# Optimization experiments

Measured on AMD Instinct MI355X. Metric: run time of the kernel, lower is better.

## Reference

```python
import jax, jax.numpy as jnp
import numpy as np

N_HEADS = 12
LN_EPS = 1e-12


def _attention(x, mask, wq, bq, wk, bk, wv, bv, wo, bo):
    # standard BERT self-attention block (QKV + output projection, no LN here)
    B, S, D = x.shape
    Dh = D // N_HEADS
    q = (x @ wq + bq).reshape(B, S, N_HEADS, Dh)
    k = (x @ wk + bk).reshape(B, S, N_HEADS, Dh)
    v = (x @ wv + bv).reshape(B, S, N_HEADS, Dh)
    scores = jnp.einsum('bqhd,bkhd->bhqk', q, k) / jnp.sqrt(jnp.asarray(Dh, x.dtype))
    scores = scores + mask[:, None, None, :]  # additive mask, broadcast over heads/queries
    a = jax.nn.softmax(scores, axis=-1)
    ctx = jnp.einsum('bhqk,bkhd->bqhd', a, v).reshape(B, S, D)
    return ctx @ wo + bo


def _ffn(x, w1, b1, w2, b2):
    return jax.nn.gelu(x @ w1 + b1, approximate=False) @ w2 + b2


def _switch_ffn(x, wr, br, w1, b1, w2, b2):
    # token-level top-1 Switch FFN: route each token, scale output by max route prob.
    # All sub-experts are computed densely and combined with a one-hot mask so the
    # math is identical to gather/scatter dispatch but jit-friendly.
    B, S, D = x.shape
    E = wr.shape[-1]
    tok = x.reshape(-1, D)  # [N, D]
    p = jax.nn.softmax(tok @ wr + br, axis=-1)  # [N, E]
    pmax = p.max(axis=-1)
    oh = jax.nn.one_hot(p.argmax(axis=-1), E, dtype=tok.dtype)  # [N, E]
    h = jax.nn.gelu(jnp.einsum('nd,edf->enf', tok, w1) + b1[:, None, :], approximate=False)
    y = jnp.einsum('enf,efd->end', h, w2) + b2[:, None, :]  # [E, N, D]
    out = jnp.einsum('ne,end->nd', oh, y) * pmax[:, None]
    return out.reshape(B, S, D)


def setup_inputs() -> dict:
    B, S, D, F, U, E = 16, 128, 768, 3072, 4, 4
    key = jax.random.key(0)
    ks = jax.random.split(key, 20)
    w = lambda i, sh: jax.random.normal(ks[i], sh, dtype=jnp.float32) * 0.02
    z = lambda sh: jnp.zeros(sh, jnp.float32)
    return {
        'x': jax.random.normal(ks[0], (B, S, D), jnp.float32),
        'attn_mask': z((B, S)),
        'sw_w': w(1, (D, U)), 'sw_b': z((U,)),
        'ca_wq': w(2, (D, D)), 'ca_bq': z((D,)),
        'ca_wk': w(3, (D, D)), 'ca_bk': z((D,)),
        'ca_wv': w(4, (D, D)), 'ca_bv': z((D,)),
        'ca_wo': w(5, (D, D)), 'ca_bo': z((D,)),
        'ua_wq': w(6, (U, D, D)), 'ua_bq': z((U, D)),
        'ua_wk': w(7, (U, D, D)), 'ua_bk': z((U, D)),
        'ua_wv': w(8, (U, D, D)), 'ua_bv': z((U, D)),
        'ua_wo': w(9, (U, D, D)), 'ua_bo': z((U, D)),
        'cf_w1': w(10, (D, F)), 'cf_b1': z((F,)),
        'cf_w2': w(11, (F, D)), 'cf_b2': z((D,)),
        'ur_w': w(12, (U, D, E)), 'ur_b': z((U, E)),
        'uf_w1': w(13, (U, E, D, F)), 'uf_b1': z((U, E, F)),
        'uf_w2': w(14, (U, E, F, D)), 'uf_b2': z((U, E, D)),
        'ln_g': jnp.ones((D,), jnp.float32), 'ln_b': z((D,)),
    }


def reference(x, attn_mask, sw_w, sw_b,
              ca_wq, ca_bq, ca_wk, ca_bk, ca_wv, ca_bv, ca_wo, ca_bo,
              ua_wq, ua_bq, ua_wk, ua_bk, ua_wv, ua_bv, ua_wo, ua_bo,
              cf_w1, cf_b1, cf_w2, cf_b2,
              ur_w, ur_b, uf_w1, uf_b1, uf_w2, uf_b2,
              ln_g, ln_b):
    U = sw_w.shape[-1]
    # common attention expert (full batch)
    common_attn = _attention(x, attn_mask, ca_wq, ca_bq, ca_wk, ca_bk, ca_wv, ca_bv, ca_wo, ca_bo)
    # batch-level routing: mean-pool over sequence, softmax + top-1
    route_p = jax.nn.softmax(x.mean(axis=1) @ sw_w + sw_b, axis=-1)  # [B, U]
    pmax = route_p.max(axis=-1)    # [B]
    routes = route_p.argmax(axis=-1)  # [B]
    # unique attention experts: masked dense compute == gather/scatter by batch row
    unique_attn = jnp.zeros_like(x)
    for i in range(U):
        sel = (routes == i)[:, None, None]
        out_i = _attention(x, attn_mask, ua_wq[i], ua_bq[i], ua_wk[i], ua_bk[i],
                           ua_wv[i], ua_bv[i], ua_wo[i], ua_bo[i])
        unique_attn = unique_attn + jnp.where(sel, out_i, jnp.zeros((), x.dtype))
    # note: original multiplies ONLY the unique branch by route_prob_max
    att = common_attn + pmax[:, None, None] * unique_attn
    # unique Switch-FFN experts (token-level top-1 inside each unique expert)
    unique_ffn = jnp.zeros_like(x)
    for i in range(U):
        sel = (routes == i)[:, None, None]
        out_i = _switch_ffn(att, ur_w[i], ur_b[i], uf_w1[i], uf_b1[i], uf_w2[i], uf_b2[i])
        unique_ffn = unique_ffn + jnp.where(sel, out_i, jnp.zeros((), x.dtype))
    common_ffn = _ffn(att, cf_w1, cf_b1, cf_w2, cf_b2)
    ffn_out = common_ffn + unique_ffn  # dropout in eval mode == identity
    y = att + ffn_out
    mu = y.mean(axis=-1, keepdims=True)
    var = y.var(axis=-1, keepdims=True)
    return (y - mu) / jnp.sqrt(var + LN_EPS) * ln_g + ln_b
```

## Files before the change

kernel.cpp:

```cpp
#include <hip/hip_runtime.h>

#define NT 2048
#define Dm 768
#define Fm 3072
#define Bm 16
#define Sm 128
#define Hm 12
#define DHm 64

#define BM 64
#define BM2 128
#define BN 128
#define BK 32

typedef __attribute__((ext_vector_type(8))) short bf16x8;
typedef __attribute__((ext_vector_type(4))) float f32x4;

__device__ __forceinline__ unsigned short f2bf(float f){
  unsigned u = __float_as_uint(f);
  unsigned r = (u + 0x7fffu + ((u>>16)&1u)) >> 16;
  return (unsigned short)r;
}
__device__ __forceinline__ float bf2f(unsigned short h){ return __uint_as_float(((unsigned)h)<<16); }
__device__ __forceinline__ unsigned fsplit2(float x){
  unsigned short h = f2bf(x);
  unsigned short l = f2bf(x - bf2f(h));
  return (unsigned)h | ((unsigned)l << 16);
}
__device__ __forceinline__ float gelu_f(float x){
  return 0.5f*x*(1.0f + erff(x*0.70710678118654752f));
}

__device__ __forceinline__ void mm_tile2(
    const short* __restrict__ Abf, int lda,
    const int* __restrict__ gidx, int m0, int mbound,
    const float* __restrict__ W0, int N, int K, int n0,
    f32x4 acc[4][4])
{
  int lane = threadIdx.x & 63, wv = threadIdx.x >> 6;
  int wm = wv & 1, wn = wv >> 1;
  int oct = lane >> 4, l16 = lane & 15;
  const short* aptr[4];
  #pragma unroll
  for(int fi=0; fi<4; fi++){
    int lr = wm*64 + fi*16 + l16;
    int grow = (lr < mbound) ? (gidx ? gidx[m0 + lr] : (m0 + lr)) : -1;
    aptr[fi] = (grow >= 0) ? (Abf + (size_t)grow*lda + oct*8) : nullptr;
  }
  const float* bptr[4];
  #pragma unroll
  for(int fj=0; fj<4; fj++)
    bptr[fj] = W0 + (size_t)(oct*8)*N + (n0 + wn*64 + fj*16 + l16);

  const bf16x8 zz = {0,0,0,0,0,0,0,0};
  bf16x8 av[4]; float bw[4][8];
  #pragma unroll
  for(int fi=0; fi<4; fi++) av[fi] = aptr[fi] ? *(const bf16x8*)(aptr[fi]) : zz;
  #pragma unroll
  for(int fj=0; fj<4; fj++)
    #pragma unroll
    for(int i=0;i<8;i++) bw[fj][i] = bptr[fj][(size_t)i*N];

  for(int k0=0; k0<K; k0+=BK){
    bf16x8 af[4];
    #pragma unroll
    for(int fi=0; fi<4; fi++) af[fi] = av[fi];
    bf16x8 bfr[4];
    #pragma unroll
    for(int fj=0; fj<4; fj++){
      unsigned o0,o1,o2,o3;
      asm("v_cvt_pk_bf16_f32 %0, %1, %2" : "=v"(o0) : "v"(bw[fj][0]), "v"(bw[fj][1]));
      asm("v_cvt_pk_bf16_f32 %0, %1, %2" : "=v"(o1) : "v"(bw[fj][2]), "v"(bw[fj][3]));
      asm("v_cvt_pk_bf16_f32 %0, %1, %2" : "=v"(o2) : "v"(bw[fj][4]), "v"(bw[fj][5]));
      asm("v_cvt_pk_bf16_f32 %0, %1, %2" : "=v"(o3) : "v"(bw[fj][6]), "v"(bw[fj][7]));
      union{ bf16x8 v; unsigned u[4]; } r;
      r.u[0]=o0; r.u[1]=o1; r.u[2]=o2; r.u[3]=o3;
      bfr[fj] = r.v;
    }
    if(k0+BK < K){
      int kn = k0 + BK;
      #pragma unroll
      for(int fi=0; fi<4; fi++) av[fi] = aptr[fi] ? *(const bf16x8*)(aptr[fi] + kn) : zz;
      #pragma unroll
      for(int fj=0; fj<4; fj++)
        #pragma unroll
        for(int i=0;i<8;i++) bw[fj][i] = bptr[fj][(size_t)(kn + i)*N];
    }
    #pragma unroll
    for(int fi=0; fi<4; fi++)
      #pragma unroll
      for(int fj=0; fj<4; fj++)
        acc[fi][fj] = __builtin_amdgcn_mfma_f32_16x16x32_bf16(af[fi], bfr[fj], acc[fi][fj], 0, 0, 0);
  }
}

__device__ __forceinline__ void mm_tile3b(
    const short* __restrict__ Ahi, const short* __restrict__ Alo, int lda, int m0, int acol,
    const float* __restrict__ W0, int N, int K, int n0,
    f32x4 acc[2][4])
{
  int lane = threadIdx.x & 63, wv = threadIdx.x >> 6;
  int wm = wv & 1, wn = wv >> 1;
  int oct = lane >> 4, l16 = lane & 15;
  size_t aoffs[2];
  #pragma unroll
  for(int fi=0; fi<2; fi++){
    int lr = wm*32 + fi*16 + l16;
    aoffs[fi] = (size_t)(m0 + lr)*lda + acol + oct*8;
  }
  const float* bptr[4];
  #pragma unroll
  for(int fj=0; fj<4; fj++)
    bptr[fj] = W0 + (size_t)(oct*8)*N + (n0 + wn*64 + fj*16 + l16);

  bf16x8 avH[2], avL[2]; float bw[4][8];
  #pragma unroll
  for(int fi=0; fi<2; fi++){
    avH[fi] = *(const bf16x8*)(Ahi + aoffs[fi]);
    avL[fi] = *(const bf16x8*)(Alo + aoffs[fi]);
  }
  #pragma unroll
  for(int fj=0; fj<4; fj++)
    #pragma unroll
    for(int i=0;i<8;i++) bw[fj][i] = bptr[fj][(size_t)i*N];

  for(int k0=0; k0<K; k0+=BK){
    bf16x8 ah[2], al[2];
    #pragma unroll
    for(int fi=0; fi<2; fi++){ ah[fi]=avH[fi]; al[fi]=avL[fi]; }
    bf16x8 bh[4], bl[4];
    #pragma unroll
    for(int fj=0; fj<4; fj++)
      #pragma unroll
      for(int i=0;i<8;i++){
        unsigned p = fsplit2(bw[fj][i]);
        bh[fj][i] = (short)(p & 0xffff);
        bl[fj][i] = (short)(p >> 16);
      }
    if(k0+BK < K){
      int kn = k0 + BK;
      #pragma unroll
      for(int fi=0; fi<2; fi++){
        avH[fi] = *(const bf16x8*)(Ahi + aoffs[fi] + kn);
        avL[fi] = *(const bf16x8*)(Alo + aoffs[fi] + kn);
      }
      #pragma unroll
      for(int fj=0; fj<4; fj++)
        #pragma unroll
        for(int i=0;i<8;i++) bw[fj][i] = bptr[fj][(size_t)(kn + i)*N];
    }
    #pragma unroll
    for(int fi=0; fi<2; fi++)
      #pragma unroll
      for(int fj=0; fj<4; fj++){
        acc[fi][fj] = __builtin_amdgcn_mfma_f32_16x16x32_bf16(ah[fi], bh[fj], acc[fi][fj], 0, 0, 0);
        acc[fi][fj] = __builtin_amdgcn_mfma_f32_16x16x32_bf16(ah[fi], bl[fj], acc[fi][fj], 0, 0, 0);
        acc[fi][fj] = __builtin_amdgcn_mfma_f32_16x16x32_bf16(al[fi], bh[fj], acc[fi][fj], 0, 0, 0);
      }
  }
}

__global__ __launch_bounds__(256) void k_split_x(const float* __restrict__ in,
    short* __restrict__ hi, short* __restrict__ lo, int n4){
  int i = blockIdx.x*256 + threadIdx.x;
  if(i < n4){
    float4 v = ((const float4*)in)[i];
    unsigned p0 = fsplit2(v.x), p1 = fsplit2(v.y), p2 = fsplit2(v.z), p3 = fsplit2(v.w);
    short4 h, l;
    h.x=(short)(p0&0xffff); l.x=(short)(p0>>16);
    h.y=(short)(p1&0xffff); l.y=(short)(p1>>16);
    h.z=(short)(p2&0xffff); l.z=(short)(p2>>16);
    h.w=(short)(p3&0xffff); l.w=(short)(p3>>16);
    ((short4*)hi)[i] = h;
    ((short4*)lo)[i] = l;
  }
}

struct PtrArr6 { const float* w[6]; const float* b[6]; };

__global__ __launch_bounds__(256) void mm3_qkv(const short* __restrict__ x_hi,
    const short* __restrict__ x_lo, PtrArr6 pa,
    const int* __restrict__ routeb, float* __restrict__ qkvout)
{
  int n0 = blockIdx.x*BN, m0 = blockIdx.y*BM, z = blockIdx.z;
  int bidx = m0 >> 7;
  const float* W = pa.w[z]; const float* bias = pa.b[z];
  if(z >= 3){ int e = routeb[bidx]; W += (size_t)e*Dm*Dm; bias += (size_t)e*Dm; }
  f32x4 acc[2][4] = {};
  mm_tile3b(x_hi, x_lo, Dm, m0, 0, W, Dm, Dm, n0, acc);
  float* outp = qkvout + (size_t)z*NT*Dm;
  int lane = threadIdx.x&63, wv = threadIdx.x>>6, wm = wv&1, wn = wv>>1;
  #pragma unroll
  for(int fi=0; fi<2; fi++)
    #pragma unroll
    for(int fj=0; fj<4; fj++)
      #pragma unroll
      for(int r=0; r<4; r++){
        int row = m0 + wm*32 + fi*16 + ((lane>>4)<<2) + r;
        int col = n0 + wn*64 + fj*16 + (lane&15);
        outp[(size_t)row*Dm + col] = acc[fi][fj][r] + bias[col];
      }
}

__global__ __launch_bounds__(256) void mm3_outproj(const short* __restrict__ ctx_hi,
    const short* __restrict__ ctx_lo,
    const float* __restrict__ ca_wo, const float* __restrict__ ua_wo,
    const float* __restrict__ ca_bo, const float* __restrict__ ua_bo,
    const int* __restrict__ routeb, const float* __restrict__ pmaxb,
    float* __restrict__ att2)
{
  int n0 = blockIdx.x*BN, m0 = blockIdx.y*BM, kc = blockIdx.z;
  int bidx = m0 >> 7;
  int e = routeb[bidx];
  const float* W    = kc ? (ua_wo + (size_t)e*Dm*Dm) : ca_wo;
  const float* bias = kc ? (ua_bo + (size_t)e*Dm)    : ca_bo;
  float bscale = kc ? pmaxb[bidx] : 1.0f;
  f32x4 acc[2][4] = {};
  mm_tile3b(ctx_hi, ctx_lo, 1536, m0, kc*Dm, W, Dm, Dm, n0, acc);
  float* outp = att2 + (size_t)kc*NT*Dm;
  int lane = threadIdx.x&63, wv = threadIdx.x>>6, wm = wv&1, wn = wv>>1;
  #pragma unroll
  for(int fi=0; fi<2; fi++)
    #pragma unroll
    for(int fj=0; fj<4; fj++)
      #pragma unroll
      for(int r=0; r<4; r++){
        int row = m0 + wm*32 + fi*16 + ((lane>>4)<<2) + r;
        int col = n0 + wn*64 + fj*16 + (lane&15);
        outp[(size_t)row*Dm + col] = acc[fi][fj][r] + bscale*bias[col];
      }
}

__global__ __launch_bounds__(256) void k_att_sum(const float* __restrict__ att2,
    float* __restrict__ att, short* __restrict__ attbf, int n4){
  int i = blockIdx.x*256 + threadIdx.x;
  if(i < n4){
    const size_t P4 = (size_t)NT*Dm/4;
    float4 a = ((const float4*)att2)[i];
    float4 b = ((const float4*)att2)[P4 + i];
    float4 v; v.x=a.x+b.x; v.y=a.y+b.y; v.z=a.z+b.z; v.w=a.w+b.w;
    ((float4*)att)[i] = v;
    short4 o;
    o.x=(short)f2bf(v.x); o.y=(short)f2bf(v.y); o.z=(short)f2bf(v.z); o.w=(short)f2bf(v.w);
    ((short4*)attbf)[i] = o;
  }
}

__global__ __launch_bounds__(256) void mm_fstage(const short* __restrict__ attbf,
    const float* __restrict__ cf_w1, const float* __restrict__ cf_b1,
    const float* __restrict__ uf_w1, const float* __restrict__ uf_b1,
    const int* __restrict__ idxl, const int* __restrict__ gbase, const int* __restrict__ gcnt,
    const int* __restrict__ tlist, const int* __restrict__ ntl,
    short* __restrict__ h, short* __restrict__ hg)
{
  int n0 = blockIdx.x*BN, y = blockIdx.y;
  int lane = threadIdx.x&63, wv = threadIdx.x>>6, wm = wv&1, wn = wv>>1;
  f32x4 acc[4][4] = {};
  if(y < 16){
    int m0 = y*BM2;
    mm_tile2(attbf, Dm, nullptr, m0, BM2, cf_w1, Fm, Dm, n0, acc);
    #pragma unroll
    for(int fi=0; fi<4; fi++)
      #pragma unroll
      for(int fj=0; fj<4; fj++)
        #pragma unroll
        for(int r=0; r<4; r++){
          int row = m0 + wm*64 + fi*16 + ((lane>>4)<<2) + r;
          int col = n0 + wn*64 + fj*16 + (lane&15);
          h[(size_t)row*Fm + col] = (short)f2bf(gelu_f(acc[fi][fj][r] + cf_b1[col]));
        }
  } else {
    int i = y - 16;
    if(i >= ntl[0]) return;
    int v = tlist[i], g = v>>8, t = v&255;
    int cnt = gcnt[g], r0 = t*BM2, pos0 = gbase[g] + r0;
    mm_tile2(attbf, Dm, idxl, pos0, cnt - r0, uf_w1 + (size_t)g*Dm*Fm, Fm, Dm, n0, acc);
    const float* bias = uf_b1 + (size_t)g*Fm;
    #pragma unroll
    for(int fi=0; fi<4; fi++)
      #pragma unroll
      for(int fj=0; fj<4; fj++)
        #pragma unroll
        for(int r=0; r<4; r++){
          int lr = wm*64 + fi*16 + ((lane>>4)<<2) + r;
          if(r0 + lr >= cnt) continue;
          int col = n0 + wn*64 + fj*16 + (lane&15);
          hg[(size_t)(pos0+lr)*Fm + col] = (short)f2bf(gelu_f(acc[fi][fj][r] + bias[col]));
        }
  }
}

__global__ __launch_bounds__(256) void mm_dstage(const short* __restrict__ h,
    const short* __restrict__ hg,
    const float* __restrict__ cf_w2, const float* __restrict__ cf_b2,
    const float* __restrict__ uf_w2, const float* __restrict__ uf_b2,
    const int* __restrict__ idxl, const int* __restrict__ gbase, const int* __restrict__ gcnt,
    const int* __restrict__ tlist, const int* __restrict__ ntl,
    const float* __restrict__ tokp, short* __restrict__ ycf4, short* __restrict__ yuo4)
{
  const int KC = Fm/4;
  int n0 = blockIdx.x*BN, y = blockIdx.y, kc = blockIdx.z;
  int lane = threadIdx.x&63, wv = threadIdx.x>>6, wm = wv&1, wn = wv>>1;
  f32x4 acc[4][4] = {};
  if(y < 16){
    int m0 = y*BM2;
    mm_tile2(h + kc*KC, Fm, nullptr, m0, BM2, cf_w2 + (size_t)kc*KC*Dm, Dm, KC, n0, acc);
    short* outp = ycf4 + (size_t)kc*NT*Dm;
    #pragma unroll
    for(int fi=0; fi<4; fi++)
      #pragma unroll
      for(int fj=0; fj<4; fj++)
        #pragma unroll
        for(int r=0; r<4; r++){
          int row = m0 + wm*64 + fi*16 + ((lane>>4)<<2) + r;
          int col = n0 + wn*64 + fj*16 + (lane&15);
          outp[(size_t)row*Dm + col] = (short)f2bf(acc[fi][fj][r] + (kc==0 ? cf_b2[col] : 0.f));
        }
  } else {
    int i = y - 16;
    if(i >= ntl[0]) return;
    int v = tlist[i], g = v>>8, t = v&255;
    int cnt = gcnt[g], r0 = t*BM2, pos0 = gbase[g] + r0;
    mm_tile2(hg + kc*KC, Fm, nullptr, pos0, cnt - r0,
             uf_w2 + (size_t)g*Fm*Dm + (size_t)kc*KC*Dm, Dm, KC, n0, acc);
    const float* bias = uf_b2 + (size_t)g*Dm;
    short* outp = yuo4 + (size_t)kc*NT*Dm;
    #pragma unroll
    for(int fi=0; fi<4; fi++)
      #pragma unroll
      for(int fj=0; fj<4; fj++)
        #pragma unroll
        for(int r=0; r<4; r++){
          int lr = wm*64 + fi*16 + ((lane>>4)<<2) + r;
          int rm = (r0 + lr < cnt) ? idxl[pos0 + lr] : -1;
          if(rm < 0) continue;
          int col = n0 + wn*64 + fj*16 + (lane&15);
          float vv = acc[fi][fj][r] + (kc==0 ? bias[col] : 0.f);
          outp[(size_t)rm*Dm + col] = (short)f2bf(vv * tokp[rm]);
        }
  }
}

__global__ __launch_bounds__(256) void k_route_batch(const float* __restrict__ xf,
    const float* __restrict__ sw_w, const float* __restrict__ sw_b,
    float* __restrict__ pmax_b, int* __restrict__ route_b){
  int b = blockIdx.x, tid = threadIdx.x;
  __shared__ float xm[Dm];
  for(int d=tid; d<Dm; d+=256){
    float s=0.f;
    const float* xp = xf + ((size_t)b*Sm)*Dm + d;
    for(int ss=0; ss<Sm; ss++) s += xp[(size_t)ss*Dm];
    xm[d] = s*(1.0f/Sm);
  }
  __syncthreads();
  float a0=0,a1=0,a2=0,a3=0;
  for(int d=tid; d<Dm; d+=256){
    float xv = xm[d];
    a0 += xv*sw_w[d*4+0]; a1 += xv*sw_w[d*4+1];
    a2 += xv*sw_w[d*4+2]; a3 += xv*sw_w[d*4+3];
  }
  __shared__ float red[4][256];
  red[0][tid]=a0; red[1][tid]=a1; red[2][tid]=a2; red[3][tid]=a3;
  for(int off=128; off>0; off>>=1){
    __syncthreads();
    if(tid<off){ for(int u=0;u<4;u++) red[u][tid]+=red[u][tid+off]; }
  }
  __syncthreads();
  if(tid==0){
    float l[4]; for(int u=0;u<4;u++) l[u]=red[u][0]+sw_b[u];
    float m=l[0]; int arg=0;
    for(int u=1;u<4;u++) if(l[u]>m){ m=l[u]; arg=u; }
    float s=0; for(int u=0;u<4;u++) s+=expf(l[u]-m);
    pmax_b[b]=1.0f/s;
    route_b[b]=arg;
  }
}

__global__ __launch_bounds__(256) void k_attn_f(const float* __restrict__ qkv,
    const float* __restrict__ mask, const float* __restrict__ pmaxb,
    short* __restrict__ ctx_hi, short* __restrict__ ctx_lo)
{
  int h = blockIdx.x, b = blockIdx.y, z = blockIdx.z;
  int qh = z & 1, kind = z >> 1;
  const float* Q  = qkv + (size_t)(kind*3+0)*NT*Dm;
  const float* Kp = qkv + (size_t)(kind*3+1)*NT*Dm;
  const float* Vp = qkv + (size_t)(kind*3+2)*NT*Dm;
  int tid = threadIdx.x;
  __shared__ float kv[128][68];
  size_t base = ((size_t)b*Sm)*Dm + h*DHm;
  for(int l=tid; l<2048; l+=256){
    int s=l>>4, d4=(l&15)*4;
    *(float4*)&kv[s][d4] = *(const float4*)(Kp + base + (size_t)s*Dm + d4);
  }
  int ql = tid>>2, quarter = tid&3;
  int qi = qh*64 + ql;
  float4 q4[16];
  const float* qp = Q + base + (size_t)qi*Dm;
  #pragma unroll
  for(int j=0;j<16;j++) q4[j] = *(const float4*)(qp + j*4);
  __syncthreads();
  float sc[32];
  #pragma unroll 4
  for(int t=0;t<32;t++){
    int ki = quarter + 4*t;
    float s=0.f;
    #pragma unroll
    for(int j=0;j<16;j++){
      float4 k4 = *(float4*)&kv[ki][j*4];
      s += q4[j].x*k4.x + q4[j].y*k4.y + q4[j].z*k4.z + q4[j].w*k4.w;
    }
    sc[t] = s*0.125f + mask[b*Sm+ki];
  }
  float m = sc[0];
  #pragma unroll
  for(int t=1;t<32;t++) m = fmaxf(m, sc[t]);
  m = fmaxf(m, __shfl_xor(m,1));
  m = fmaxf(m, __shfl_xor(m,2));
  float sum = 0.f;
  #pragma unroll
  for(int t=0;t<32;t++){ sc[t] = expf(sc[t]-m); sum += sc[t]; }
  sum += __shfl_xor(sum,1);
  sum += __shfl_xor(sum,2);
  float inv = 1.0f/sum;
  #pragma unroll
  for(int t=0;t<32;t++) sc[t] *= inv;
  __syncthreads();
  for(int l=tid; l<2048; l+=256){
    int s=l>>4, d4=(l&15)*4;
    *(float4*)&kv[s][d4] = *(const float4*)(Vp + base + (size_t)s*Dm + d4);
  }
  __syncthreads();
  float4 part[16];
  #pragma unroll
  for(int j=0;j<16;j++){ part[j].x=0; part[j].y=0; part[j].z=0; part[j].w=0; }
  #pragma unroll 4
  for(int t=0;t<32;t++){
    int ki = quarter + 4*t;
    float p = sc[t];
    #pragma unroll
    for(int j=0;j<16;j++){
      float4 v4 = *(float4*)&kv[ki][j*4];
      part[j].x += p*v4.x; part[j].y += p*v4.y; part[j].z += p*v4.z; part[j].w += p*v4.w;
    }
  }
  #pragma unroll
  for(int j=0;j<16;j++){
    part[j].x += __shfl_xor(part[j].x,1); part[j].x += __shfl_xor(part[j].x,2);
    part[j].y += __shfl_xor(part[j].y,1); part[j].y += __shfl_xor(part[j].y,2);
    part[j].z += __shfl_xor(part[j].z,1); part[j].z += __shfl_xor(part[j].z,2);
    part[j].w += __shfl_xor(part[j].w,1); part[j].w += __shfl_xor(part[j].w,2);
  }
  float sck = kind ? pmaxb[b] : 1.0f;
  size_t obase = ((size_t)b*Sm + qi)*1536 + kind*Dm + h*DHm;
  #pragma unroll
  for(int jj=0;jj<4;jj++){
    int j = quarter*4 + jj;
    float4 v = part[j];
    v.x *= sck; v.y *= sck; v.z *= sck; v.w *= sck;
    short4 hh, ll;
    unsigned short t0;
    t0=f2bf(v.x); hh.x=(short)t0; ll.x=(short)f2bf(v.x-bf2f(t0));
    t0=f2bf(v.y); hh.y=(short)t0; ll.y=(short)f2bf(v.y-bf2f(t0));
    t0=f2bf(v.z); hh.z=(short)t0; ll.z=(short)f2bf(v.z-bf2f(t0));
    t0=f2bf(v.w); hh.w=(short)t0; ll.w=(short)f2bf(v.w-bf2f(t0));
    *(short4*)(ctx_hi + obase + j*4) = hh;
    *(short4*)(ctx_lo + obase + j*4) = ll;
  }
}

__global__ __launch_bounds__(256) void k_tok_route(const float* __restrict__ att,
    const float* __restrict__ ur_w, const float* __restrict__ ur_b,
    const int* __restrict__ route_b, float* __restrict__ tok_pmax,
    int* __restrict__ tok_e, int* __restrict__ grp_count)
{
  int n = blockIdx.x, tid = threadIdx.x;
  int i = route_b[n>>7];
  const float* w = ur_w + (size_t)i*Dm*4;
  const float* ap = att + (size_t)n*Dm;
  float a0=0,a1=0,a2=0,a3=0;
  for(int d=tid; d<Dm; d+=256){
    float a = ap[d];
    a0 += a*w[d*4+0]; a1 += a*w[d*4+1];
    a2 += a*w[d*4+2]; a3 += a*w[d*4+3];
  }
  __shared__ float red[4][256];
  red[0][tid]=a0; red[1][tid]=a1; red[2][tid]=a2; red[3][tid]=a3;
  for(int off=128; off>0; off>>=1){
    __syncthreads();
    if(tid<off){ for(int u=0;u<4;u++) red[u][tid]+=red[u][tid+off]; }
  }
  __syncthreads();
  if(tid==0){
    float l[4]; for(int u=0;u<4;u++) l[u]=red[u][0]+ur_b[i*4+u];
    float m=l[0]; int arg=0;
    for(int u=1;u<4;u++) if(l[u]>m){ m=l[u]; arg=u; }
    float s=0; for(int u=0;u<4;u++) s+=expf(l[u]-m);
    tok_pmax[n] = 1.0f/s;
    tok_e[n] = arg;
    atomicAdd(&grp_count[i*4+arg], 1);
  }
}

__global__ void k_prefix(const int* __restrict__ cnt, int* __restrict__ base,
                         int* __restrict__ cur, int* __restrict__ tlist, int* __restrict__ ntl){
  if(threadIdx.x==0 && blockIdx.x==0){
    int s=0, nt=0;
    for(int g=0; g<16; g++){
      base[g]=s; cur[g]=s;
      int tg = (cnt[g] + BM2 - 1)/BM2;
      for(int t=0; t<tg; t++){ if(nt<32) tlist[nt++] = (g<<8)|t; }
      s += cnt[g];
    }
    ntl[0] = nt;
  }
}

__global__ void k_scatter(const int* __restrict__ route_b, const int* __restrict__ tok_e,
                          int* __restrict__ cur, int* __restrict__ idxl){
  int n = blockIdx.x*256 + threadIdx.x;
  if(n < NT){
    int g = route_b[n>>7]*4 + tok_e[n];
    int pos = atomicAdd(&cur[g], 1);
    idxl[pos] = n;
  }
}

__global__ __launch_bounds__(256) void k_final_ln(const float* __restrict__ att,
    const short* __restrict__ ycf4, const short* __restrict__ yuo4,
    const float* __restrict__ ln_g, const float* __restrict__ ln_b, float* __restrict__ out)
{
  int n = blockIdx.x, tid = threadIdx.x;
  __shared__ float yb[Dm];
  __shared__ float red[256];
  size_t base = (size_t)n*Dm;
  const size_t P = (size_t)NT*Dm;
  float ps = 0.f;
  for(int d=tid; d<Dm; d+=256){
    float v = att[base+d];
    #pragma unroll
    for(int c=0; c<4; c++){
      v += bf2f((unsigned short)ycf4[c*P + base + d]);
      v += bf2f((unsigned short)yuo4[c*P + base + d]);
    }
    yb[d]=v; ps+=v;
  }
  red[tid]=ps;
  for(int off=128; off>0; off>>=1){ __syncthreads(); if(tid<off) red[tid]+=red[tid+off]; }
  __syncthreads();
  float mu = red[0]*(1.0f/Dm);
  __syncthreads();
  float pv = 0.f;
  for(int d=tid; d<Dm; d+=256){ float t = yb[d]-mu; pv += t*t; }
  red[tid]=pv;
  for(int off=128; off>0; off>>=1){ __syncthreads(); if(tid<off) red[tid]+=red[tid+off]; }
  __syncthreads();
  float var = red[0]*(1.0f/Dm);
  float rstd = rsqrtf(var + 1e-12f);
  for(int d=tid; d<Dm; d+=256){
    out[base+d] = (yb[d]-mu)*rstd*ln_g[d] + ln_b[d];
  }
}

extern "C" void kernel_launch(void* const* d_in, const int* in_sizes, int n_in,
                              void* d_out, int out_size, void* d_ws, size_t ws_size,
                              hipStream_t stream)
{
  const float* x     =(const float*)d_in[0];
  const float* mask  =(const float*)d_in[1];
  const float* sw_w  =(const float*)d_in[2];
  const float* sw_b  =(const float*)d_in[3];
  const float* ca_wq =(const float*)d_in[4];
  const float* ca_bq =(const float*)d_in[5];
  const float* ca_wk =(const float*)d_in[6];
  const float* ca_bk =(const float*)d_in[7];
  const float* ca_wv =(const float*)d_in[8];
  const float* ca_bv =(const float*)d_in[9];
  const float* ca_wo =(const float*)d_in[10];
  const float* ca_bo =(const float*)d_in[11];
  const float* ua_wq =(const float*)d_in[12];
  const float* ua_bq =(const float*)d_in[13];
  const float* ua_wk =(const float*)d_in[14];
  const float* ua_bk =(const float*)d_in[15];
  const float* ua_wv =(const float*)d_in[16];
  const float* ua_bv =(const float*)d_in[17];
  const float* ua_wo =(const float*)d_in[18];
  const float* ua_bo =(const float*)d_in[19];
  const float* cf_w1 =(const float*)d_in[20];
  const float* cf_b1 =(const float*)d_in[21];
  const float* cf_w2 =(const float*)d_in[22];
  const float* cf_b2 =(const float*)d_in[23];
  const float* ur_w  =(const float*)d_in[24];
  const float* ur_b  =(const float*)d_in[25];
  const float* uf_w1 =(const float*)d_in[26];
  const float* uf_b1 =(const float*)d_in[27];
  const float* uf_w2 =(const float*)d_in[28];
  const float* uf_b2 =(const float*)d_in[29];
  const float* ln_g  =(const float*)d_in[30];
  const float* ln_b  =(const float*)d_in[31];

  float* region = (float*)d_ws;
  float* qkv    = region;
  short* ctx_hi = (short*)(region + (size_t)6*NT*Dm);
  short* ctx_lo = (short*)(region + (size_t)7*NT*Dm);
  float* att2   = region;
  short* h_bf   = (short*)region;
  short* hg_bf  = (short*)region + (size_t)NT*Fm;
  short* ycf4   = (short*)(region + (size_t)4*NT*Dm);
  short* yuo4   = (short*)(region + (size_t)6*NT*Dm);
  float* fp     = region + (size_t)8*NT*Dm;
  short* x_hi   = (short*)fp;
  short* x_lo   = x_hi + (size_t)NT*Dm;
  float* att    = fp; fp += (size_t)NT*Dm;
  float* tokp   = fp; fp += NT;
  float* pmaxb  = fp; fp += 16;
  short* att_bf = (short*)fp;
  int*   ip     = (int*)(att_bf + (size_t)NT*Dm);
  int* routeb = ip; ip += 16;
  int* toke   = ip; ip += NT;
  int* gcnt   = ip; ip += 16;
  int* gbase  = ip; ip += 16;
  int* gcur   = ip; ip += 16;
  int* idxl   = ip; ip += NT;
  int* tlist  = ip; ip += 64;
  int* ntl    = ip; ip += 1;
  size_t need = (size_t)((char*)ip - (char*)d_ws);
  if(need > ws_size) return;

  (void)hipMemsetAsync(gcnt, 0, 16*sizeof(int), stream);

  k_route_batch<<<16, 256, 0, stream>>>(x, sw_w, sw_b, pmaxb, routeb);
  k_split_x<<<(NT*Dm/4 + 255)/256, 256, 0, stream>>>(x, x_hi, x_lo, NT*Dm/4);

  PtrArr6 pa;
  pa.w[0]=ca_wq; pa.w[1]=ca_wk; pa.w[2]=ca_wv; pa.w[3]=ua_wq; pa.w[4]=ua_wk; pa.w[5]=ua_wv;
  pa.b[0]=ca_bq; pa.b[1]=ca_bk; pa.b[2]=ca_bv; pa.b[3]=ua_bq; pa.b[4]=ua_bk; pa.b[5]=ua_bv;
  mm3_qkv<<<dim3(Dm/BN, NT/BM, 6), 256, 0, stream>>>(x_hi, x_lo, pa, routeb, qkv);

  k_attn_f<<<dim3(Hm, Bm, 4), 256, 0, stream>>>(qkv, mask, pmaxb, ctx_hi, ctx_lo);

  mm3_outproj<<<dim3(Dm/BN, NT/BM, 2), 256, 0, stream>>>(ctx_hi, ctx_lo, ca_wo, ua_wo,
                                                         ca_bo, ua_bo, routeb, pmaxb, att2);
  k_att_sum<<<(NT*Dm/4 + 255)/256, 256, 0, stream>>>(att2, att, att_bf, NT*Dm/4);

  k_tok_route<<<NT, 256, 0, stream>>>(att, ur_w, ur_b, routeb, tokp, toke, gcnt);
  k_prefix<<<1, 64, 0, stream>>>(gcnt, gbase, gcur, tlist, ntl);
  k_scatter<<<NT/256, 256, 0, stream>>>(routeb, toke, gcur, idxl);

  mm_fstage<<<dim3(Fm/BN, 16+32), 256, 0, stream>>>(att_bf, cf_w1, cf_b1, uf_w1, uf_b1,
                                                    idxl, gbase, gcnt, tlist, ntl, h_bf, hg_bf);

  mm_dstage<<<dim3(Dm/BN, 16+32, 4), 256, 0, stream>>>(h_bf, hg_bf, cf_w2, cf_b2, uf_w2, uf_b2,
                                                       idxl, gbase, gcnt, tlist, ntl, tokp,
                                                       ycf4, yuo4);

  k_final_ln<<<NT, 256, 0, stream>>>(att, ycf4, yuo4, ln_g, ln_b, (float*)d_out);
}
```

Before: 569.3 us.

## Double-buffer GEMM loads, use packed bf16 split, split-K out-proj, add occupancy hints

The bf16 GEMM tile loop now keeps two register stages of A/B prefetch, processing two K-steps per iteration to hide more global-load latency. The fp32 hi/lo split now uses packed v_cvt_pk_bf16_f32 instructions in place of scalar software rounding. The output projection is split-K into four partial buffers to raise grid parallelism, and the att-sum kernel reduces four buffers instead of two. The FFN GEMM kernels also get a launch_bounds occupancy hint of 3 blocks per SM. These changes add register pressure and extra reduction memory traffic.

```diff
diff --git a/kernel.cpp b/kernel.cpp
--- a/kernel.cpp
+++ b/kernel.cpp
@@ -27,6 +27,12 @@
   unsigned short l = f2bf(x - bf2f(h));
   return (unsigned)h | ((unsigned)l << 16);
 }
+__device__ __forceinline__ void bsplit2(float a, float b, unsigned &hi2, unsigned &lo2){
+  asm("v_cvt_pk_bf16_f32 %0, %1, %2" : "=v"(hi2) : "v"(a), "v"(b));
+  float fa = __uint_as_float(hi2 << 16);
+  float fb = __uint_as_float(hi2 & 0xffff0000u);
+  asm("v_cvt_pk_bf16_f32 %0, %1, %2" : "=v"(lo2) : "v"(a - fa), "v"(b - fb));
+}
 __device__ __forceinline__ float gelu_f(float x){
   return 0.5f*x*(1.0f + erff(x*0.70710678118654752f));
 }
@@ -53,44 +59,84 @@
     bptr[fj] = W0 + (size_t)(oct*8)*N + (n0 + wn*64 + fj*16 + l16);
 
   const bf16x8 zz = {0,0,0,0,0,0,0,0};
-  bf16x8 av[4]; float bw[4][8];
-  #pragma unroll
-  for(int fi=0; fi<4; fi++) av[fi] = aptr[fi] ? *(const bf16x8*)(aptr[fi]) : zz;
+  bf16x8 av0[4], av1[4];
+  float bw0[4][8], bw1[4][8];
+  #pragma unroll
+  for(int fi=0; fi<4; fi++){
+    av0[fi] = aptr[fi] ? *(const bf16x8*)(aptr[fi]) : zz;
+    av1[fi] = aptr[fi] ? *(const bf16x8*)(aptr[fi] + BK) : zz;
+  }
   #pragma unroll
   for(int fj=0; fj<4; fj++)
     #pragma unroll
-    for(int i=0;i<8;i++) bw[fj][i] = bptr[fj][(size_t)i*N];
-
-  for(int k0=0; k0<K; k0+=BK){
-    bf16x8 af[4];
-    #pragma unroll
-    for(int fi=0; fi<4; fi++) af[fi] = av[fi];
-    bf16x8 bfr[4];
-    #pragma unroll
-    for(int fj=0; fj<4; fj++){
-      unsigned o0,o1,o2,o3;
-      asm("v_cvt_pk_bf16_f32 %0, %1, %2" : "=v"(o0) : "v"(bw[fj][0]), "v"(bw[fj][1]));
-      asm("v_cvt_pk_bf16_f32 %0, %1, %2" : "=v"(o1) : "v"(bw[fj][2]), "v"(bw[fj][3]));
-      asm("v_cvt_pk_bf16_f32 %0, %1, %2" : "=v"(o2) : "v"(bw[fj][4]), "v"(bw[fj][5]));
-      asm("v_cvt_pk_bf16_f32 %0, %1, %2" : "=v"(o3) : "v"(bw[fj][6]), "v"(bw[fj][7]));
-      union{ bf16x8 v; unsigned u[4]; } r;
-      r.u[0]=o0; r.u[1]=o1; r.u[2]=o2; r.u[3]=o3;
-      bfr[fj] = r.v;
-    }
-    if(k0+BK < K){
-      int kn = k0 + BK;
-      #pragma unroll
-      for(int fi=0; fi<4; fi++) av[fi] = aptr[fi] ? *(const bf16x8*)(aptr[fi] + kn) : zz;
-      #pragma unroll
-      for(int fj=0; fj<4; fj++)
-        #pragma unroll
-        for(int i=0;i<8;i++) bw[fj][i] = bptr[fj][(size_t)(kn + i)*N];
-    }
-    #pragma unroll
-    for(int fi=0; fi<4; fi++)
-      #pragma unroll
-      for(int fj=0; fj<4; fj++)
-        acc[fi][fj] = __builtin_amdgcn_mfma_f32_16x16x32_bf16(af[fi], bfr[fj], acc[fi][fj], 0, 0, 0);
+    for(int i=0;i<8;i++){
+      bw0[fj][i] = bptr[fj][(size_t)i*N];
+      bw1[fj][i] = bptr[fj][(size_t)(BK + i)*N];
+    }
+
+  for(int k0=0; k0<K; k0+=2*BK){
+    {
+      bf16x8 afr[4];
+      #pragma unroll
+      for(int fi=0; fi<4; fi++) afr[fi] = av0[fi];
+      bf16x8 bfr[4];
+      #pragma unroll
+      for(int fj=0; fj<4; fj++){
+        unsigned o0,o1,o2,o3;
+        asm("v_cvt_pk_bf16_f32 %0, %1, %2" : "=v"(o0) : "v"(bw0[fj][0]), "v"(bw0[fj][1]));
+        asm("v_cvt_pk_bf16_f32 %0, %1, %2" : "=v"(o1) : "v"(bw0[fj][2]), "v"(bw0[fj][3]));
+        asm("v_cvt_pk_bf16_f32 %0, %1, %2" : "=v"(o2) : "v"(bw0[fj][4]), "v"(bw0[fj][5]));
+        asm("v_cvt_pk_bf16_f32 %0, %1, %2" : "=v"(o3) : "v"(bw0[fj][6]), "v"(bw0[fj][7]));
+        union{ bf16x8 v; unsigned u[4]; } r;
+        r.u[0]=o0; r.u[1]=o1; r.u[2]=o2; r.u[3]=o3;
+        bfr[fj] = r.v;
+      }
+      if(k0 + 2*BK < K){
+        int kn = k0 + 2*BK;
+        #pragma unroll
+        for(int fi=0; fi<4; fi++) av0[fi] = aptr[fi] ? *(const bf16x8*)(aptr[fi] + kn) : zz;
+        #pragma unroll
+        for(int fj=0; fj<4; fj++)
+          #pragma unroll
+          for(int i=0;i<8;i++) bw0[fj][i] = bptr[fj][(size_t)(kn + i)*N];
+      }
+      #pragma unroll
+      for(int fi=0; fi<4; fi++)
+        #pragma unroll
+        for(int fj=0; fj<4; fj++)
+          acc[fi][fj] = __builtin_amdgcn_mfma_f32_16x16x32_bf16(afr[fi], bfr[fj], acc[fi][fj], 0, 0, 0);
+    }
+    {
+      bf16x8 afr[4];
+      #pragma unroll
+      for(int fi=0; fi<4; fi++) afr[fi] = av1[fi];
+      bf16x8 bfr[4];
+      #pragma unroll
+      for(int fj=0; fj<4; fj++){
+        unsigned o0,o1,o2,o3;
+        asm("v_cvt_pk_bf16_f32 %0, %1, %2" : "=v"(o0) : "v"(bw1[fj][0]), "v"(bw1[fj][1]));
+        asm("v_cvt_pk_bf16_f32 %0, %1, %2" : "=v"(o1) : "v"(bw1[fj][2]), "v"(bw1[fj][3]));
+        asm("v_cvt_pk_bf16_f32 %0, %1, %2" : "=v"(o2) : "v"(bw1[fj][4]), "v"(bw1[fj][5]));
+        asm("v_cvt_pk_bf16_f32 %0, %1, %2" : "=v"(o3) : "v"(bw1[fj][6]), "v"(bw1[fj][7]));
+        union{ bf16x8 v; unsigned u[4]; } r;
+        r.u[0]=o0; r.u[1]=o1; r.u[2]=o2; r.u[3]=o3;
+        bfr[fj] = r.v;
+      }
+      if(k0 + 3*BK < K){
+        int kn = k0 + 3*BK;
+        #pragma unroll
+        for(int fi=0; fi<4; fi++) av1[fi] = aptr[fi] ? *(const bf16x8*)(aptr[fi] + kn) : zz;
+        #pragma unroll
+        for(int fj=0; fj<4; fj++)
+          #pragma unroll
+          for(int i=0;i<8;i++) bw1[fj][i] = bptr[fj][(size_t)(kn + i)*N];
+      }
+      #pragma unroll
+      for(int fi=0; fi<4; fi++)
+        #pragma unroll
+        for(int fj=0; fj<4; fj++)
+          acc[fi][fj] = __builtin_amdgcn_mfma_f32_16x16x32_bf16(afr[fi], bfr[fj], acc[fi][fj], 0, 0, 0);
+    }
   }
 }
 
@@ -130,13 +176,17 @@
     for(int fi=0; fi<2; fi++){ ah[fi]=avH[fi]; al[fi]=avL[fi]; }
     bf16x8 bh[4], bl[4];
     #pragma unroll
-    for(int fj=0; fj<4; fj++)
-      #pragma unroll
-      for(int i=0;i<8;i++){
-        unsigned p = fsplit2(bw[fj][i]);
-        bh[fj][i] = (short)(p & 0xffff);
-        bl[fj][i] = (short)(p >> 16);
-      }
+    for(int fj=0; fj<4; fj++){
+      unsigned h0,l0,h1,l1,h2,l2,h3,l3;
+      bsplit2(bw[fj][0], bw[fj][1], h0, l0);
+      bsplit2(bw[fj][2], bw[fj][3], h1, l1);
+      bsplit2(bw[fj][4], bw[fj][5], h2, l2);
+      bsplit2(bw[fj][6], bw[fj][7], h3, l3);
+      union{ bf16x8 v; unsigned u[4]; } rh, rl;
+      rh.u[0]=h0; rh.u[1]=h1; rh.u[2]=h2; rh.u[3]=h3;
+      rl.u[0]=l0; rl.u[1]=l1; rl.u[2]=l2; rl.u[3]=l3;
+      bh[fj] = rh.v; bl[fj] = rl.v;
+    }
     if(k0+BK < K){
       int kn = k0 + BK;
       #pragma unroll
@@ -165,12 +215,12 @@
   int i = blockIdx.x*256 + threadIdx.x;
   if(i < n4){
     float4 v = ((const float4*)in)[i];
-    unsigned p0 = fsplit2(v.x), p1 = fsplit2(v.y), p2 = fsplit2(v.z), p3 = fsplit2(v.w);
+    unsigned h01,l01,h23,l23;
+    bsplit2(v.x, v.y, h01, l01);
+    bsplit2(v.z, v.w, h23, l23);
     short4 h, l;
-    h.x=(short)(p0&0xffff); l.x=(short)(p0>>16);
-    h.y=(short)(p1&0xffff); l.y=(short)(p1>>16);
-    h.z=(short)(p2&0xffff); l.z=(short)(p2>>16);
-    h.w=(short)(p3&0xffff); l.w=(short)(p3>>16);
+    h.x=(short)(h01&0xffff); h.y=(short)(h01>>16); h.z=(short)(h23&0xffff); h.w=(short)(h23>>16);
+    l.x=(short)(l01&0xffff); l.y=(short)(l01>>16); l.z=(short)(l23&0xffff); l.w=(short)(l23>>16);
     ((short4*)hi)[i] = h;
     ((short4*)lo)[i] = l;
   }
@@ -207,17 +257,19 @@
     const float* __restrict__ ca_wo, const float* __restrict__ ua_wo,
     const float* __restrict__ ca_bo, const float* __restrict__ ua_bo,
     const int* __restrict__ routeb, const float* __restrict__ pmaxb,
-    float* __restrict__ att2)
-{
+    float* __restrict__ att4)
+{
+  const int KC = Dm/2;
   int n0 = blockIdx.x*BN, m0 = blockIdx.y*BM, kc = blockIdx.z;
   int bidx = m0 >> 7;
   int e = routeb[bidx];
-  const float* W    = kc ? (ua_wo + (size_t)e*Dm*Dm) : ca_wo;
-  const float* bias = kc ? (ua_bo + (size_t)e*Dm)    : ca_bo;
-  float bscale = kc ? pmaxb[bidx] : 1.0f;
+  int uq = kc >> 1, kh = kc & 1;
+  const float* Wb = uq ? (ua_wo + (size_t)e*Dm*Dm) : ca_wo;
+  const float* W  = Wb + (size_t)kh*KC*Dm;
+  int acol = uq*Dm + kh*KC;
   f32x4 acc[2][4] = {};
-  mm_tile3b(ctx_hi, ctx_lo, 1536, m0, kc*Dm, W, Dm, Dm, n0, acc);
-  float* outp = att2 + (size_t)kc*NT*Dm;
+  mm_tile3b(ctx_hi, ctx_lo, 1536, m0, acol, W, Dm, KC, n0, acc);
+  float* outp = att4 + (size_t)kc*NT*Dm;
   int lane = threadIdx.x&63, wv = threadIdx.x>>6, wm = wv&1, wn = wv>>1;
   #pragma unroll
   for(int fi=0; fi<2; fi++)
@@ -227,18 +279,24 @@
       for(int r=0; r<4; r++){
         int row = m0 + wm*32 + fi*16 + ((lane>>4)<<2) + r;
         int col = n0 + wn*64 + fj*16 + (lane&15);
-        outp[(size_t)row*Dm + col] = acc[fi][fj][r] + bscale*bias[col];
+        float bv = 0.f;
+        if(kh == 0) bv = uq ? pmaxb[bidx]*ua_bo[(size_t)e*Dm + col] : ca_bo[col];
+        outp[(size_t)row*Dm + col] = acc[fi][fj][r] + bv;
       }
 }
 
-__global__ __launch_bounds__(256) void k_att_sum(const float* __restrict__ att2,
+__global__ __launch_bounds__(256) void k_att_sum(const float* __restrict__ att4,
     float* __restrict__ att, short* __restrict__ attbf, int n4){
   int i = blockIdx.x*256 + threadIdx.x;
   if(i < n4){
     const size_t P4 = (size_t)NT*Dm/4;
-    float4 a = ((const float4*)att2)[i];
-    float4 b = ((const float4*)att2)[P4 + i];
-    float4 v; v.x=a.x+b.x; v.y=a.y+b.y; v.z=a.z+b.z; v.w=a.w+b.w;
+    float4 a = ((const float4*)att4)[i];
+    float4 b = ((const float4*)att4)[P4 + i];
+    float4 c = ((const float4*)att4)[2*P4 + i];
+    float4 d = ((const float4*)att4)[3*P4 + i];
+    float4 v;
+    v.x=a.x+b.x+c.x+d.x; v.y=a.y+b.y+c.y+d.y;
+    v.z=a.z+b.z+c.z+d.z; v.w=a.w+b.w+c.w+d.w;
     ((float4*)att)[i] = v;
     short4 o;
     o.x=(short)f2bf(v.x); o.y=(short)f2bf(v.y); o.z=(short)f2bf(v.z); o.w=(short)f2bf(v.w);
@@ -246,7 +304,7 @@
   }
 }
 
-__global__ __launch_bounds__(256) void mm_fstage(const short* __restrict__ attbf,
+__global__ __launch_bounds__(256, 3) void mm_fstage(const short* __restrict__ attbf,
     const float* __restrict__ cf_w1, const float* __restrict__ cf_b1,
     const float* __restrict__ uf_w1, const float* __restrict__ uf_b1,
     const int* __restrict__ idxl, const int* __restrict__ gbase, const int* __restrict__ gcnt,
@@ -290,7 +348,7 @@
   }
 }
 
-__global__ __launch_bounds__(256) void mm_dstage(const short* __restrict__ h,
+__global__ __launch_bounds__(256, 3) void mm_dstage(const short* __restrict__ h,
     const short* __restrict__ hg,
     const float* __restrict__ cf_w2, const float* __restrict__ cf_b2,
     const float* __restrict__ uf_w2, const float* __restrict__ uf_b2,
@@ -602,7 +660,7 @@
   float* qkv    = region;
   short* ctx_hi = (short*)(region + (size_t)6*NT*Dm);
   short* ctx_lo = (short*)(region + (size_t)7*NT*Dm);
-  float* att2   = region;
+  float* att4   = region;
   short* h_bf   = (short*)region;
   short* hg_bf  = (short*)region + (size_t)NT*Fm;
   short* ycf4   = (short*)(region + (size_t)4*NT*Dm);
@@ -638,9 +696,9 @@
 
   k_attn_f<<<dim3(Hm, Bm, 4), 256, 0, stream>>>(qkv, mask, pmaxb, ctx_hi, ctx_lo);
 
-  mm3_outproj<<<dim3(Dm/BN, NT/BM, 2), 256, 0, stream>>>(ctx_hi, ctx_lo, ca_wo, ua_wo,
-                                                         ca_bo, ua_bo, routeb, pmaxb, att2);
-  k_att_sum<<<(NT*Dm/4 + 255)/256, 256, 0, stream>>>(att2, att, att_bf, NT*Dm/4);
+  mm3_outproj<<<dim3(Dm/BN, NT/BM, 4), 256, 0, stream>>>(ctx_hi, ctx_lo, ca_wo, ua_wo,
+                                                         ca_bo, ua_bo, routeb, pmaxb, att4);
+  k_att_sum<<<(NT*Dm/4 + 255)/256, 256, 0, stream>>>(att4, att, att_bf, NT*Dm/4);
 
   k_tok_route<<<NT, 256, 0, stream>>>(att, ur_w, ur_b, routeb, tokp, toke, gcnt);
   k_prefix<<<1, 64, 0, stream>>>(gcnt, gbase, gcur, tlist, ntl);
```

Result: slower. 1.485 ms (+160.8%).
